# Kernel tuning notes

Measured on AMD Instinct MI355X. Metric: run time of the kernel, lower is better.

Reference implementation:

```python
import jax, jax.numpy as jnp
import numpy as np

EPS = 1e-7
BLOCK_SIZE = 128
LN_EPS = 1e-6

def _project(x):
    norm = jnp.maximum(jnp.linalg.norm(x, axis=-1, keepdims=True), EPS)
    max_norm = 1.0 - EPS
    return jnp.where(norm >= 1.0, x / norm * max_norm, x)

def _mobius_add(x, y, c):
    x2 = jnp.sum(x * x, -1, keepdims=True)
    y2 = jnp.sum(y * y, -1, keepdims=True)
    xy = jnp.sum(x * y, -1, keepdims=True)
    num = (1 + 2 * c * xy + c * y2) * x + (1 - c * x2) * y
    den = 1 + 2 * c * xy + c * c * x2 * y2
    return _project(num / jnp.maximum(den, EPS))

def _logmap0(y, c):
    sqrt_c = jnp.maximum(jnp.sqrt(c), EPS)
    y_norm = jnp.linalg.norm(y, axis=-1, keepdims=True)
    safe = jnp.maximum(y_norm, EPS)
    mag = jnp.arctanh(jnp.minimum(y_norm, 1.0 - EPS)) / sqrt_c
    return jnp.where(y_norm < EPS, jnp.zeros_like(y), mag * (y / safe))

def _expmap0(v, c):
    sqrt_c = jnp.maximum(jnp.sqrt(c), EPS)
    v_norm = jnp.linalg.norm(v, axis=-1, keepdims=True)
    safe = jnp.maximum(v_norm, EPS)
    mag = jnp.tanh(sqrt_c * safe) / sqrt_c
    return _project(jnp.where(v_norm < EPS, jnp.zeros_like(v), mag * (v / safe)))

def _dist(x, y, c):
    sqrt_c = jnp.maximum(jnp.sqrt(c), EPS)
    add_norm = jnp.linalg.norm(_mobius_add(-x, y, c), axis=-1)
    sc = jnp.squeeze(sqrt_c, -1)
    arg = jnp.minimum(sc * add_norm, 1.0 - EPS)
    return 2.0 * jnp.arctanh(arg) / sc

def _layernorm(t, scale, bias):
    mu = jnp.mean(t, -1, keepdims=True)
    var = jnp.mean((t - mu) ** 2, -1, keepdims=True)
    return (t - mu) * jax.lax.rsqrt(var + LN_EPS) * scale + bias

def _rope(x, fc):
    # x: [Be, H, bs, hd]; fc: [bs, hd//2] complex
    x_r, x_i = jnp.split(x, 2, -1)
    xc = jax.lax.complex(x_r, x_i)
    rot = xc * fc.reshape(1, 1, fc.shape[0], fc.shape[1])
    return jnp.concatenate([rot.real, rot.imag], -1)

def setup_inputs() -> dict:
    key = jax.random.key(0)
    ks = jax.random.split(key, 8)
    B, N, D, H = 1, 1024, 1024, 16
    w = lambda k, s: jax.random.normal(k, s, jnp.float32) * 0.02
    x = jax.random.normal(ks[0], (B, N, D), jnp.float32) * 0.02  # points inside the ball
    c_global = jax.random.uniform(ks[1], (B, 1), jnp.float32, minval=0.1, maxval=1.0)
    return dict(
        x=x, c_global=c_global,
        qkv_w=w(ks[2], (D, 3 * D)), qkv_b=jnp.zeros((3 * D,), jnp.float32),
        out_w=w(ks[3], (D, D)), out_b=jnp.zeros((D,), jnp.float32),
        ffn_w1=w(ks[4], (D, 4 * D)), ffn_b1=jnp.zeros((4 * D,), jnp.float32),
        ffn_w2=w(ks[5], (4 * D, D)), ffn_b2=jnp.zeros((D,), jnp.float32),
        ln1_scale=jnp.ones((D,), jnp.float32), ln1_bias=jnp.zeros((D,), jnp.float32),
        ln2_scale=jnp.ones((D,), jnp.float32), ln2_bias=jnp.zeros((D,), jnp.float32),
        c_logits=jnp.zeros((H,), jnp.float32),
        geo_scale=jnp.ones((1, H, 1, 1), jnp.float32),
        start_pos=0,
    )

def reference(x, c_global, qkv_w, qkv_b, out_w, out_b, ffn_w1, ffn_b1, ffn_w2, ffn_b2,
              ln1_scale, ln1_bias, ln2_scale, ln2_bias, c_logits, geo_scale, start_pos):
    B, N, D = x.shape
    H = c_logits.shape[0]
    hd = D // H
    bs = BLOCK_SIZE
    nb = N // bs
    Be = B * nb
    xb = x.reshape(Be, bs, D)
    c_b = jnp.repeat(c_global, nb, axis=0).reshape(Be, 1, 1)
    x_res1 = xb
    # tangent-space norm 1 + attention input
    x_norm = _expmap0(_layernorm(_logmap0(xb, c_b), ln1_scale, ln1_bias), c_b)
    x_tan = _logmap0(x_norm, c_b)
    qkv = (x_tan @ qkv_w + qkv_b).reshape(Be, bs, 3, H, hd).transpose(2, 0, 3, 1, 4)
    q, k, v = qkv[0], qkv[1], qkv[2]  # [Be, H, bs, hd]
    # block-local RoPE (module recomputes freqs_cis for h_dim/block_size internally)
    freqs = 1.0 / (10000.0 ** (jnp.arange(0, hd, 2, dtype=jnp.float32) / hd))
    fc = jnp.exp(1j * jnp.outer(jnp.arange(bs), freqs))
    q = _rope(q, fc)
    k = _rope(k, fc)
    c_head = jax.nn.softplus(c_logits).reshape(1, H, 1, 1)
    q_hyp = _expmap0(q, c_head)
    k_hyp = _expmap0(k, c_head)
    d = _dist(q_hyp[:, :, :, None, :], k_hyp[:, :, None, :, :], c_head[:, :, None, :, :])  # [Be,H,bs,bs]
    attn = jax.nn.softmax(-geo_scale * d, axis=-1)
    ao = jnp.einsum('bhqk,bhkd->bhqd', attn, v).transpose(0, 2, 1, 3).reshape(Be, bs, D)
    ao = ao @ out_w + out_b
    x_att = _mobius_add(x_res1, _expmap0(ao, c_b), c_b)
    # tangent-space norm 2 + hyperbolic FFN
    x_norm2 = _expmap0(_layernorm(_logmap0(x_att, c_b), ln2_scale, ln2_bias), c_b)
    t = _logmap0(x_norm2, c_b)
    t = jax.nn.gelu(t @ ffn_w1 + ffn_b1) @ ffn_w2 + ffn_b2
    x_ffn = _expmap0(t, c_b)
    out = _mobius_add(x_att, x_ffn, c_b)
    return out.reshape(B, N, D)
```

## Files before the change

kernel.cpp:

```cpp
#include <hip/hip_runtime.h>

typedef unsigned int uint;
typedef unsigned short ushort;
typedef __attribute__((ext_vector_type(8))) short bf16x8;
typedef __attribute__((ext_vector_type(4))) float f32x4;

#define EPSF 1e-7f
#define ONE_M_EPS 0.99999988079071044921875f
#define ATANH_1ME 8.4056213f
#define Y2_CLIP 0.99999982f

__device__ __forceinline__ ushort f2bf(float f){
  union{float f;uint u;}x; x.f=f; uint u=x.u;
  return (ushort)((u + 0x7fffu + ((u>>16)&1u)) >> 16);
}
__device__ __forceinline__ float bf2f(ushort u){
  union{uint u;float f;}x; x.u = ((uint)u)<<16; return x.f;
}
__device__ __forceinline__ float atanh_c(float a){
  a = fminf(a, ONE_M_EPS);
  return 0.5f*__logf((1.f+a)/(1.f-a));
}
__device__ __forceinline__ float gelu_t(float v){
  return 0.5f*v*(1.f + tanhf(0.7978845608f*(v + 0.044715f*v*v*v)));
}

__device__ __forceinline__ float expmap_factor(float n2, float sc, float& r2){
  float n = sqrtf(n2);
  if (n < EPSF) { r2 = 0.f; return 0.f; }
  float mag = tanhf(sc*n)/sc;
  float f = mag/n;
  if (mag >= 1.f) { f *= ONE_M_EPS/mag; r2 = Y2_CLIP; }
  else r2 = mag*mag;
  return f;
}
__device__ __forceinline__ float roundtrip_factor(float tn2, float sc){
  float tn = sqrtf(tn2);
  if (tn < EPSF) return 0.f;
  float mag = tanhf(sc*tn)/sc;
  if (mag >= 1.f) {
    return ATANH_1ME / (sc * tn);
  } else {
    if (mag < EPSF) return 0.f;
    return (mag/tn) * (atanh_c(mag) / (sc * mag));
  }
}

__device__ __constant__ float FREQS[32] = {
  1.0f, 0.7498942093324559f, 0.5623413251903491f, 0.4216965034285822f,
  0.31622776601683794f, 0.23713737056616552f, 0.1778279410038923f, 0.13335214321633242f,
  0.1f, 0.07498942093324558f, 0.05623413251903491f, 0.04216965034285822f,
  0.03162277660168379f, 0.023713737056616554f, 0.01778279410038923f, 0.013335214321633242f,
  0.01f, 0.007498942093324559f, 0.005623413251903491f, 0.004216965034285822f,
  0.0031622776601683794f, 0.0023713737056616554f, 0.0017782794100389228f, 0.0013335214321633241f,
  0.001f, 0.0007498942093324558f, 0.0005623413251903491f, 0.0004216965034285822f,
  0.00031622776601683794f, 0.00023713737056616553f, 0.00017782794100389227f, 0.00013335214321633243f
};

__device__ __forceinline__ float blkSum(float v, float* tmp){
  #pragma unroll
  for (int o=32;o>0;o>>=1) v += __shfl_xor(v, o, 64);
  int w = threadIdx.x >> 6;
  if ((threadIdx.x & 63) == 0) tmp[w] = v;
  __syncthreads();
  v = tmp[0]+tmp[1]+tmp[2]+tmp[3];
  __syncthreads();
  return v;
}
__device__ __forceinline__ float2 blkSum2(float a, float b, float* tmp){
  #pragma unroll
  for (int o=32;o>0;o>>=1){ a += __shfl_xor(a, o, 64); b += __shfl_xor(b, o, 64); }
  int w = threadIdx.x >> 6;
  if ((threadIdx.x & 63) == 0){ tmp[w] = a; tmp[4+w] = b; }
  __syncthreads();
  float2 r; r.x = tmp[0]+tmp[1]+tmp[2]+tmp[3]; r.y = tmp[4]+tmp[5]+tmp[6]+tmp[7];
  __syncthreads();
  return r;
}

__global__ __launch_bounds__(256) void k_pre(const float* __restrict__ qkv_w,
    const float* __restrict__ out_w, const float* __restrict__ ffn_w1,
    const float* __restrict__ ffn_w2, const float* __restrict__ x,
    const float* __restrict__ cg, const float* __restrict__ lns, const float* __restrict__ lnb,
    ushort* __restrict__ wq, ushort* __restrict__ wo,
    ushort* __restrict__ w1, ushort* __restrict__ w2, ushort* __restrict__ xtan){
  __shared__ float s[32][33];
  int b = blockIdx.x;
  if (b < 12288){
    const float* W; ushort* WT; int K, N;
    if (b < 3072){ W=qkv_w; WT=wq; K=1024; N=3072; }
    else if (b < 4096){ b-=3072; W=out_w; WT=wo; K=1024; N=1024; }
    else if (b < 8192){ b-=4096; W=ffn_w1; WT=w1; K=1024; N=4096; }
    else { b-=8192; W=ffn_w2; WT=w2; K=4096; N=1024; }
    int nbn = N >> 5;
    int n0 = (b % nbn)*32, k0 = (b / nbn)*32;
    int tx = threadIdx.x & 31, ty = threadIdx.x >> 5;
    #pragma unroll
    for (int i=0;i<4;i++)
      s[ty+8*i][tx] = W[(size_t)(k0+ty+8*i)*N + n0+tx];
    __syncthreads();
    #pragma unroll
    for (int i=0;i<4;i++)
      WT[(size_t)(n0+ty+8*i)*K + k0+tx] = f2bf(s[tx][ty+8*i]);
  } else {
    float* tmp = &s[0][0];
    int r = b - 12288, t = threadIdx.x;
    float c = cg[0];
    float sc = fmaxf(sqrtf(c), EPSF);
    float4 xv = ((const float4*)(x + (size_t)r*1024))[t];
    float n2 = blkSum(xv.x*xv.x + xv.y*xv.y + xv.z*xv.z + xv.w*xv.w, tmp);
    float n = sqrtf(n2);
    float f1 = (n < EPSF) ? 0.f : (atanh_c(n) / sc / n);
    float ux = xv.x*f1, uy = xv.y*f1, uz = xv.z*f1, uw = xv.w*f1;
    float2 s12 = blkSum2(ux+uy+uz+uw, ux*ux+uy*uy+uz*uz+uw*uw, tmp);
    float mu = s12.x*(1.f/1024.f);
    float var = s12.y*(1.f/1024.f) - mu*mu;
    float inv = rsqrtf(var + 1e-6f);
    float4 sv = ((const float4*)lns)[t];
    float4 bv = ((const float4*)lnb)[t];
    float ta = (ux-mu)*inv*sv.x + bv.x;
    float tb = (uy-mu)*inv*sv.y + bv.y;
    float tc = (uz-mu)*inv*sv.z + bv.z;
    float td = (uw-mu)*inv*sv.w + bv.w;
    float tn2 = blkSum(ta*ta+tb*tb+tc*tc+td*td, tmp);
    float f = roundtrip_factor(tn2, sc);
    ushort4 o; o.x=f2bf(ta*f); o.y=f2bf(tb*f); o.z=f2bf(tc*f); o.w=f2bf(td*f);
    ((ushort4*)(xtan + (size_t)r*1024))[t] = o;
  }
}

template<int EPI>
__global__ __launch_bounds__(256) void k_gemm(const ushort* __restrict__ A,
    const ushort* __restrict__ Bt, const float* __restrict__ bias,
    void* __restrict__ C, int M, int N, int Kstride, int Kchunk){
  constexpr int NF = 4;
  __shared__ ushort As[2][64*64];
  __shared__ ushort Bs[2][64*64];
  const int tid = threadIdx.x;
  const int lane = tid & 63;
  const int wid = tid >> 6;
  const int ro = wid * 16;
  const int l15 = lane & 15, hi = lane >> 4;
  const int nwg = gridDim.x * gridDim.y;
  const int lin = blockIdx.y * gridDim.x + blockIdx.x;
  const int qq = nwg >> 3, rr = nwg & 7;
  const int xcd = lin & 7, ii = lin >> 3;
  const int swz = (xcd < rr) ? (xcd*(qq+1) + ii) : (rr*(qq+1) + (xcd-rr)*qq + ii);
  const int m0 = (swz % gridDim.y) * 64;
  const int n0 = (swz / gridDim.y) * 64;
  const int z = blockIdx.z;
  const int kbase = z * Kchunk;
  const int swr = (l15 & 7) << 3;

  f32x4 acc[NF];
  #pragma unroll
  for (int j=0;j<NF;j++) acc[j] = (f32x4){0.f,0.f,0.f,0.f};

  auto stage = [&](int buf, int koff){
    #pragma unroll
    for (int r2=0;r2<2;r2++){
      int idx = r2*256 + tid;
      int row = idx >> 3, cc = idx & 7;
      int off = koff + ((cc ^ (row & 7)) << 3);
      int lo = (r2*256 + (tid & 192)) * 8;
      __builtin_amdgcn_global_load_lds((const __attribute__((address_space(1))) uint*)
          (A + (size_t)(m0+row)*Kstride + off),
          (__attribute__((address_space(3))) uint*)&As[buf][lo], 16, 0, 0);
      __builtin_amdgcn_global_load_lds((const __attribute__((address_space(1))) uint*)
          (Bt + (size_t)(n0+row)*Kstride + off),
          (__attribute__((address_space(3))) uint*)&Bs[buf][lo], 16, 0, 0);
    }
  };
  auto compute = [&](int buf){
    #pragma unroll
    for (int ks=0;ks<2;ks++){
      bf16x8 af, bfv[NF];
      int cb = (ks*32 + hi*8) ^ swr;
      af = *(const bf16x8*)&As[buf][(ro+l15)*64 + cb];
      #pragma unroll
      for (int n2=0;n2<NF;n2++) bfv[n2] = *(const bf16x8*)&Bs[buf][(n2*16+l15)*64 + cb];
      #pragma unroll
      for (int n2=0;n2<NF;n2++)
        acc[n2] = __builtin_amdgcn_mfma_f32_16x16x32_bf16(af, bfv[n2], acc[n2], 0, 0, 0);
    }
  };

  const int nt = Kchunk >> 6;
  stage(0, kbase);
  __syncthreads();
  int cur = 0;
  for (int t = 1; t < nt; ++t){
    stage(cur ^ 1, kbase + t*64);
    compute(cur);
    __syncthreads();
    cur ^= 1;
  }
  compute(cur);

  #pragma unroll
  for (int n=0;n<NF;n++){
    int gc = n0 + n*16 + l15;
    float bb = (EPI == 3) ? (z == 0 ? bias[gc] : 0.f) : bias[gc];
    #pragma unroll
    for (int i=0;i<4;i++){
      int gr = m0 + ro + hi*4 + i;
      float v = acc[n][i] + bb;
      if (EPI == 2) v = gelu_t(v);
      if (EPI == 2) ((ushort*)C)[(size_t)gr*N + gc] = f2bf(v);
      else ((float*)C)[(size_t)z*M*N + (size_t)gr*N + gc] = v;
    }
  }
}

__global__ __launch_bounds__(256) void k_qkvprep(const float* __restrict__ qkv,
    const float* __restrict__ clog,
    ushort* __restrict__ qhg, ushort* __restrict__ qlg,
    ushort* __restrict__ khg, ushort* __restrict__ klg,
    ushort* __restrict__ vhg, float* __restrict__ q2g, float* __restrict__ k2g){
  const int gr = blockIdx.x;
  const int be = gr >> 7, r = gr & 127;
  const int t = threadIdx.x;
  const int h = t >> 4, d = t & 15;
  const float cl = clog[h];
  const float ch = (cl > 20.f) ? cl : log1pf(__expf(cl));
  const float sc = fmaxf(sqrtf(ch), EPSF);
  const float* base = qkv + (size_t)gr*3072 + h*64;
  const size_t rowbase = ((size_t)(be*16 + h)*128 + r)*64;
  const float fr = (float)r;
  #pragma unroll
  for (int qk=0; qk<2; qk++){
    int off = qk*1024;
    float v0 = base[off+d];
    float v1 = base[off+d+16];
    float v2 = base[off+d+32];
    float v3 = base[off+d+48];
    float sn, cn;
    __sincosf(fr * FREQS[d], &sn, &cn);
    float a = v0, b = v2;
    v0 = a*cn - b*sn; v2 = a*sn + b*cn;
    __sincosf(fr * FREQS[d+16], &sn, &cn);
    a = v1; b = v3;
    v1 = a*cn - b*sn; v3 = a*sn + b*cn;
    float n2 = v0*v0 + v1*v1 + v2*v2 + v3*v3;
    #pragma unroll
    for (int o=1;o<16;o<<=1) n2 += __shfl_xor(n2, o);
    float r2; float f = expmap_factor(n2, sc, r2);
    ushort* hd = qk ? khg : qhg;
    ushort* ld = qk ? klg : qlg;
    float val;
    val = v0*f; ushort h0 = f2bf(val), l0 = f2bf(val - bf2f(h0));
    val = v1*f; ushort h1 = f2bf(val), l1 = f2bf(val - bf2f(h1));
    val = v2*f; ushort h2 = f2bf(val), l2 = f2bf(val - bf2f(h2));
    val = v3*f; ushort h3 = f2bf(val), l3 = f2bf(val - bf2f(h3));
    hd[rowbase+d]=h0; hd[rowbase+d+16]=h1; hd[rowbase+d+32]=h2; hd[rowbase+d+48]=h3;
    ld[rowbase+d]=l0; ld[rowbase+d+16]=l1; ld[rowbase+d+32]=l2; ld[rowbase+d+48]=l3;
    if (d == 0) (qk ? k2g : q2g)[(size_t)(be*16+h)*128 + r] = r2;
  }
  {
    vhg[rowbase+d]    = f2bf(base[2048+d]);
    vhg[rowbase+d+16] = f2bf(base[2048+d+16]);
    vhg[rowbase+d+32] = f2bf(base[2048+d+32]);
    vhg[rowbase+d+48] = f2bf(base[2048+d+48]);
  }
}

__global__ __launch_bounds__(256) void k_attn6(const ushort* __restrict__ qhg,
    const ushort* __restrict__ qlg, const ushort* __restrict__ khg,
    const ushort* __restrict__ klg, const ushort* __restrict__ vhg,
    const float* __restrict__ q2g, const float* __restrict__ k2g,
    const float* __restrict__ c_logits, const float* __restrict__ geo,
    ushort* __restrict__ ao){
  __shared__ ushort Kh[128*64], Kl[128*64];
  __shared__ ushort Vth[64*128];
  __shared__ ushort Qh[64*64], Ql[64*64];
  __shared__ float k2s[128], q2s[64];
  const int h = blockIdx.x, be = blockIdx.y, qs = blockIdx.z;
  const int tid = threadIdx.x;
  const float cl = c_logits[h];
  const float ch = (cl > 20.f) ? cl : log1pf(__expf(cl));
  const float sc = fmaxf(sqrtf(ch), EPSF);
  const float gs = geo[h];
  const size_t tbase = (size_t)(be*16 + h)*8192;

  #pragma unroll
  for (int r2=0;r2<4;r2++){
    int idx = r2*256 + tid;
    int row = idx >> 3, cc = idx & 7;
    int off = row*64 + ((cc ^ (row & 7)) << 3);
    int lo = (r2*256 + (tid & 192)) * 8;
    __builtin_amdgcn_global_load_lds((const __attribute__((address_space(1))) uint*)(khg + tbase + off),
        (__attribute__((address_space(3))) uint*)&Kh[lo], 16, 0, 0);
    __builtin_amdgcn_global_load_lds((const __attribute__((address_space(1))) uint*)(klg + tbase + off),
        (__attribute__((address_space(3))) uint*)&Kl[lo], 16, 0, 0);
  }
  #pragma unroll
  for (int r2=0;r2<2;r2++){
    int idx = r2*256 + tid;
    int row = idx >> 3, cc = idx & 7;
    int off = (qs*64 + row)*64 + ((cc ^ (row & 7)) << 3);
    int lo = (r2*256 + (tid & 192)) * 8;
    __builtin_amdgcn_global_load_lds((const __attribute__((address_space(1))) uint*)(qhg + tbase + off),
        (__attribute__((address_space(3))) uint*)&Qh[lo], 16, 0, 0);
    __builtin_amdgcn_global_load_lds((const __attribute__((address_space(1))) uint*)(qlg + tbase + off),
        (__attribute__((address_space(3))) uint*)&Ql[lo], 16, 0, 0);
  }
  if (tid < 128){
    int kv = tid;
    const uint4* src = (const uint4*)(vhg + tbase + kv*64);
    ushort v[64];
    #pragma unroll
    for (int c2=0;c2<8;c2++) *(uint4*)&v[c2*8] = src[c2];
    #pragma unroll
    for (int d=0; d<64; d++){
      int idx = d*128 + (((kv>>3) ^ (d&7))<<3) + (kv&7);
      Vth[idx] = v[d];
    }
    k2s[kv] = k2g[(size_t)(be*16+h)*128 + kv];
  } else if (tid < 192){
    int i2 = tid - 128;
    q2s[i2] = q2g[(size_t)(be*16+h)*128 + qs*64 + i2];
  }
  __syncthreads();

  const int lane = tid & 63, w = tid >> 6;
  const int l15 = lane & 15, hi4 = lane >> 4;
  f32x4 acc[8];
  #pragma unroll
  for (int nf=0;nf<8;nf++) acc[nf] = (f32x4){0.f,0.f,0.f,0.f};
  #pragma unroll
  for (int ks=0; ks<2; ks++){
    int qrowL = w*16 + l15;
    int qidx = qrowL*64 + (((ks*4 + hi4) ^ (qrowL&7))<<3);
    bf16x8 qh = *(const bf16x8*)&Qh[qidx];
    bf16x8 ql2 = *(const bf16x8*)&Ql[qidx];
    #pragma unroll
    for (int nf=0; nf<8; nf++){
      int krow = nf*16 + l15;
      int kidx = krow*64 + (((ks*4 + hi4) ^ (krow&7))<<3);
      bf16x8 kh = *(const bf16x8*)&Kh[kidx];
      bf16x8 kl2 = *(const bf16x8*)&Kl[kidx];
      acc[nf] = __builtin_amdgcn_mfma_f32_16x16x32_bf16(qh, kh, acc[nf], 0, 0, 0);
      acc[nf] = __builtin_amdgcn_mfma_f32_16x16x32_bf16(qh, kl2, acc[nf], 0, 0, 0);
      acc[nf] = __builtin_amdgcn_mfma_f32_16x16x32_bf16(ql2, kh, acc[nf], 0, 0, 0);
    }
  }
  __syncthreads();

  float q2v[4], Bfv[4];
  #pragma unroll
  for (int i=0;i<4;i++){ q2v[i] = q2s[w*16 + hi4*4 + i]; Bfv[i] = 1.f - ch*q2v[i]; }
  const float e2 = 2.f*ch;
  #pragma unroll
  for (int nf=0; nf<8; nf++){
    float k2 = k2s[nf*16 + l15];
    #pragma unroll
    for (int i=0;i<4;i++){
      float xy = acc[nf][i];
      float Af = 1.f + ch*k2 - e2*xy;
      float den = fmaxf(Af - ch*k2*Bfv[i], EPSF);
      float num2 = fmaxf(Af*(Af*q2v[i] - 2.f*Bfv[i]*xy) + Bfv[i]*Bfv[i]*k2, 0.f);
      float rn = sqrtf(num2)/den;
      rn = (rn >= 1.f) ? ONE_M_EPS : rn;
      float arg = fminf(sc*rn, ONE_M_EPS);
      float dd = __logf((1.f+arg)/(1.f-arg)) / sc;
      acc[nf][i] = -gs*dd;
    }
  }
  #pragma unroll
  for (int i=0;i<4;i++){
    float m = acc[0][i];
    #pragma unroll
    for (int nf=1;nf<8;nf++) m = fmaxf(m, acc[nf][i]);
    #pragma unroll
    for (int o=1;o<16;o<<=1) m = fmaxf(m, __shfl_xor(m, o));
    float l = 0.f;
    #pragma unroll
    for (int nf=0;nf<8;nf++){ float pp = __expf(acc[nf][i]-m); acc[nf][i] = pp; l += pp; }
    #pragma unroll
    for (int o=1;o<16;o<<=1) l += __shfl_xor(l, o);
    float inv = 1.f/l;
    #pragma unroll
    for (int nf=0;nf<8;nf++){
      float p = acc[nf][i]*inv;
      ushort ph = f2bf(p);
      ushort pl = f2bf(p - bf2f(ph));
      int row = w*16 + hi4*4 + i, col = nf*16 + l15;
      int idx = row*128 + (((col>>3) ^ (row&7))<<3) + (col&7);
      Kh[idx] = ph; Kl[idx] = pl;
    }
  }
  __syncthreads();

  f32x4 acc2[4];
  #pragma unroll
  for (int nf=0;nf<4;nf++) acc2[nf] = (f32x4){0.f,0.f,0.f,0.f};
  #pragma unroll
  for (int ks=0; ks<4; ks++){
    int prow = w*16 + l15;
    int pidx = prow*128 + (((ks*4 + hi4) ^ (prow&7))<<3);
    bf16x8 ph = *(const bf16x8*)&Kh[pidx];
    bf16x8 pl = *(const bf16x8*)&Kl[pidx];
    #pragma unroll
    for (int nf=0; nf<4; nf++){
      int vrow = nf*16 + l15;
      int vidx = vrow*128 + (((ks*4 + hi4) ^ (vrow&7))<<3);
      bf16x8 vh = *(const bf16x8*)&Vth[vidx];
      acc2[nf] = __builtin_amdgcn_mfma_f32_16x16x32_bf16(ph, vh, acc2[nf], 0, 0, 0);
      acc2[nf] = __builtin_amdgcn_mfma_f32_16x16x32_bf16(pl, vh, acc2[nf], 0, 0, 0);
    }
  }
  #pragma unroll
  for (int nf=0; nf<4; nf++)
    #pragma unroll
    for (int i=0;i<4;i++){
      int row = qs*64 + w*16 + hi4*4 + i;
      int col = nf*16 + l15;
      ao[(size_t)(be*128 + row)*1024 + h*64 + col] = f2bf(acc2[nf][i]);
    }
}

__global__ __launch_bounds__(256) void k_postattn(const float* __restrict__ x,
    const float* __restrict__ proj, const float* __restrict__ cg,
    const float* __restrict__ lns, const float* __restrict__ lnb,
    float* __restrict__ xatt, ushort* __restrict__ tout){
  __shared__ float tmp[8];
  int r = blockIdx.x, t = threadIdx.x;
  float c = cg[0], sc = fmaxf(sqrtf(c), EPSF);
  float4 pa = ((const float4*)(proj + (size_t)r*1024))[t];
  float4 pb = ((const float4*)(proj + 1024*1024 + (size_t)r*1024))[t];
  float4 pc = ((const float4*)(proj + 2*1024*1024 + (size_t)r*1024))[t];
  float4 pd = ((const float4*)(proj + 3*1024*1024 + (size_t)r*1024))[t];
  float4 pv; pv.x=(pa.x+pb.x)+(pc.x+pd.x); pv.y=(pa.y+pb.y)+(pc.y+pd.y);
  pv.z=(pa.z+pb.z)+(pc.z+pd.z); pv.w=(pa.w+pb.w)+(pc.w+pd.w);
  float4 xv = ((const float4*)(x + (size_t)r*1024))[t];
  float pn2 = blkSum(pv.x*pv.x+pv.y*pv.y+pv.z*pv.z+pv.w*pv.w, tmp);
  float y2; float fy = expmap_factor(pn2, sc, y2);
  float ya = pv.x*fy, yb = pv.y*fy, yc = pv.z*fy, yd = pv.w*fy;
  float2 s = blkSum2(xv.x*xv.x+xv.y*xv.y+xv.z*xv.z+xv.w*xv.w,
                     xv.x*ya+xv.y*yb+xv.z*yc+xv.w*yd, tmp);
  float x2 = s.x, xy = s.y;
  float Af = 1.f + 2.f*c*xy + c*y2;
  float Bf = 1.f - c*x2;
  float den = fmaxf(1.f + 2.f*c*xy + c*c*x2*y2, EPSF);
  float num2 = fmaxf(Af*Af*x2 + 2.f*Af*Bf*xy + Bf*Bf*y2, 0.f);
  float rn = sqrtf(num2)/den;
  float fp = (rn >= 1.f) ? (ONE_M_EPS/fmaxf(rn,EPSF)) : 1.f;
  float xan = (rn >= 1.f) ? ONE_M_EPS : rn;
  float g = fp/den;
  float xa = (Af*xv.x + Bf*ya)*g;
  float xb = (Af*xv.y + Bf*yb)*g;
  float xc = (Af*xv.z + Bf*yc)*g;
  float xd = (Af*xv.w + Bf*yd)*g;
  float4 xo; xo.x=xa; xo.y=xb; xo.z=xc; xo.w=xd;
  ((float4*)(xatt + (size_t)r*1024))[t] = xo;
  float at = (rn >= 1.f) ? ATANH_1ME : atanh_c(xan);
  float fl = (xan < EPSF) ? 0.f : at / sc / fmaxf(xan, EPSF);
  float ux = xa*fl, uy = xb*fl, uz = xc*fl, uw = xd*fl;
  float2 s12 = blkSum2(ux+uy+uz+uw, ux*ux+uy*uy+uz*uz+uw*uw, tmp);
  float mu = s12.x*(1.f/1024.f);
  float var = s12.y*(1.f/1024.f) - mu*mu;
  float inv = rsqrtf(var + 1e-6f);
  float4 sv = ((const float4*)lns)[t];
  float4 bv = ((const float4*)lnb)[t];
  float ta = (ux-mu)*inv*sv.x + bv.x;
  float tb = (uy-mu)*inv*sv.y + bv.y;
  float tc = (uz-mu)*inv*sv.z + bv.z;
  float td = (uw-mu)*inv*sv.w + bv.w;
  float tn2 = blkSum(ta*ta+tb*tb+tc*tc+td*td, tmp);
  float f = roundtrip_factor(tn2, sc);
  ushort4 o; o.x=f2bf(ta*f); o.y=f2bf(tb*f); o.z=f2bf(tc*f); o.w=f2bf(td*f);
  ((ushort4*)(tout + (size_t)r*1024))[t] = o;
}

__global__ __launch_bounds__(256) void k_final(const float* __restrict__ xatt,
    const float* __restrict__ tf, const float* __restrict__ cg, float* __restrict__ out){
  __shared__ float tmp[8];
  int r = blockIdx.x, t = threadIdx.x;
  float c = cg[0], sc = fmaxf(sqrtf(c), EPSF);
  float4 fa = ((const float4*)(tf + (size_t)r*1024))[t];
  float4 fb = ((const float4*)(tf + 1024*1024 + (size_t)r*1024))[t];
  float4 fc = ((const float4*)(tf + 2*1024*1024 + (size_t)r*1024))[t];
  float4 fd = ((const float4*)(tf + 3*1024*1024 + (size_t)r*1024))[t];
  float4 fv; fv.x=(fa.x+fb.x)+(fc.x+fd.x); fv.y=(fa.y+fb.y)+(fc.y+fd.y);
  fv.z=(fa.z+fb.z)+(fc.z+fd.z); fv.w=(fa.w+fb.w)+(fc.w+fd.w);
  float4 xv = ((const float4*)(xatt + (size_t)r*1024))[t];
  float fn2 = blkSum(fv.x*fv.x+fv.y*fv.y+fv.z*fv.z+fv.w*fv.w, tmp);
  float y2; float fy = expmap_factor(fn2, sc, y2);
  float ya = fv.x*fy, yb = fv.y*fy, yc = fv.z*fy, yd = fv.w*fy;
  float2 s = blkSum2(xv.x*xv.x+xv.y*xv.y+xv.z*xv.z+xv.w*xv.w,
                     xv.x*ya+xv.y*yb+xv.z*yc+xv.w*yd, tmp);
  float x2 = s.x, xy = s.y;
  float Af = 1.f + 2.f*c*xy + c*y2;
  float Bf = 1.f - c*x2;
  float den = fmaxf(1.f + 2.f*c*xy + c*c*x2*y2, EPSF);
  float num2 = fmaxf(Af*Af*x2 + 2.f*Af*Bf*xy + Bf*Bf*y2, 0.f);
  float rn = sqrtf(num2)/den;
  float fp = (rn >= 1.f) ? (ONE_M_EPS/fmaxf(rn,EPSF)) : 1.f;
  float g = fp/den;
  float4 o;
  o.x = (Af*xv.x + Bf*ya)*g;
  o.y = (Af*xv.y + Bf*yb)*g;
  o.z = (Af*xv.z + Bf*yc)*g;
  o.w = (Af*xv.w + Bf*yd)*g;
  ((float4*)(out + (size_t)r*1024))[t] = o;
}

extern "C" void kernel_launch(void* const* d_in, const int* in_sizes, int n_in,
                              void* d_out, int out_size, void* d_ws, size_t ws_size,
                              hipStream_t stream){
  (void)in_sizes; (void)n_in; (void)out_size; (void)ws_size;
  const float* x     = (const float*)d_in[0];
  const float* cg    = (const float*)d_in[1];
  const float* qkv_w = (const float*)d_in[2];
  const float* qkv_b = (const float*)d_in[3];
  const float* out_w = (const float*)d_in[4];
  const float* out_b = (const float*)d_in[5];
  const float* ffn_w1= (const float*)d_in[6];
  const float* ffn_b1= (const float*)d_in[7];
  const float* ffn_w2= (const float*)d_in[8];
  const float* ffn_b2= (const float*)d_in[9];
  const float* ln1s  = (const float*)d_in[10];
  const float* ln1b  = (const float*)d_in[11];
  const float* ln2s  = (const float*)d_in[12];
  const float* ln2b  = (const float*)d_in[13];
  const float* clog  = (const float*)d_in[14];
  const float* geo   = (const float*)d_in[15];

  char* p = (char*)d_ws;
  auto take = [&](size_t n){ char* r = p; p += (n + 255) & ~(size_t)255; return r; };
  ushort* wt_qkv  = (ushort*)take((size_t)3072*1024*2);
  ushort* wt_out  = (ushort*)take((size_t)1024*1024*2);
  ushort* wt_ffn1 = (ushort*)take((size_t)4096*1024*2);
  ushort* wt_ffn2 = (ushort*)take((size_t)1024*4096*2);
  float*  bufA    = (float*)take((size_t)1024*3072*4);
  ushort* bufB    = (ushort*)take((size_t)1024*1024*2);
  float*  bufC    = (float*)take((size_t)4*1024*1024*4);
  float*  xatt    = (float*)take((size_t)1024*1024*4);
  ushort* tbuf    = (ushort*)take((size_t)1024*1024*2);
  ushort* qhg     = (ushort*)take((size_t)1024*1024*2);
  ushort* qlg     = (ushort*)take((size_t)1024*1024*2);
  ushort* khg     = (ushort*)take((size_t)1024*1024*2);
  ushort* klg     = (ushort*)take((size_t)1024*1024*2);
  ushort* vhg     = (ushort*)take((size_t)1024*1024*2);
  float*  q2g     = (float*)take((size_t)16384*4);
  float*  k2g     = (float*)take((size_t)16384*4);

  k_pre<<<13312, 256, 0, stream>>>(qkv_w, out_w, ffn_w1, ffn_w2, x, cg, ln1s, ln1b,
                                   wt_qkv, wt_out, wt_ffn1, wt_ffn2, bufB);
  k_gemm<3><<<dim3(48,16,1), 256, 0, stream>>>(bufB, wt_qkv, qkv_b, (void*)bufA, 1024, 3072, 1024, 1024);
  k_qkvprep<<<1024, 256, 0, stream>>>(bufA, clog, qhg, qlg, khg, klg, vhg, q2g, k2g);
  k_attn6<<<dim3(16,8,2), 256, 0, stream>>>(qhg, qlg, khg, klg, vhg, q2g, k2g, clog, geo, bufB);
  k_gemm<3><<<dim3(16,16,4), 256, 0, stream>>>(bufB, wt_out, out_b, (void*)bufC, 1024, 1024, 1024, 256);
  k_postattn<<<1024, 256, 0, stream>>>(x, bufC, cg, ln2s, ln2b, xatt, tbuf);
  k_gemm<2><<<dim3(64,16,1), 256, 0, stream>>>(tbuf, wt_ffn1, ffn_b1, (void*)bufA, 1024, 4096, 1024, 1024);
  k_gemm<3><<<dim3(16,16,4), 256, 0, stream>>>((const ushort*)bufA, wt_ffn2, ffn_b2, (void*)bufC, 1024, 1024, 4096, 1024);
  k_final<<<1024, 256, 0, stream>>>(xatt, bufC, cg, (float*)d_out);
}
```

Baseline: 113.3 us.

## Fuse QKV RoPE/expmap/bf16 split epilogue into QKV GEMM, drop qkvprep kernel

Adds a GEMM epilogue variant that applies RoPE, the expmap0 scaling, the hi/lo bf16 split and the head-major scatter directly from the accumulators, then deletes the separate k_qkvprep kernel. This avoids writing and re-reading the 12 MB fp32 QKV intermediate and saves one kernel launch. In exchange the GEMM epilogue gets heavier, with per-row sincos and cross-lane shuffles, and its scattered 2-byte stores may coalesce poorly. The bufA allocation is enlarged, though that does not appear needed for this path.

```diff
diff --git a/kernel.cpp b/kernel.cpp
--- a/kernel.cpp
+++ b/kernel.cpp
@@ -132,7 +132,11 @@
 template<int EPI>
 __global__ __launch_bounds__(256) void k_gemm(const ushort* __restrict__ A,
     const ushort* __restrict__ Bt, const float* __restrict__ bias,
-    void* __restrict__ C, int M, int N, int Kstride, int Kchunk){
+    void* __restrict__ C, int M, int N, int Kstride, int Kchunk,
+    ushort* __restrict__ qhg = nullptr, ushort* __restrict__ qlg = nullptr,
+    ushort* __restrict__ khg = nullptr, ushort* __restrict__ klg = nullptr,
+    ushort* __restrict__ vhg = nullptr, float* __restrict__ q2g = nullptr,
+    float* __restrict__ k2g = nullptr, const float* __restrict__ clog = nullptr){
   constexpr int NF = 4;
   __shared__ ushort As[2][64*64];
   __shared__ ushort Bs[2][64*64];
@@ -197,6 +201,64 @@
   }
   compute(cur);
 
+  if (EPI == 4){
+    const int type = n0 >> 10;
+    const int h = (n0 & 1023) >> 6;
+    float v[NF][4];
+    #pragma unroll
+    for (int n2=0;n2<NF;n2++){
+      float bb = bias[n0 + n2*16 + l15];
+      #pragma unroll
+      for (int i=0;i<4;i++) v[n2][i] = acc[n2][i] + bb;
+    }
+    if (type < 2){
+      const float cl = clog[h];
+      const float chh = (cl > 20.f) ? cl : log1pf(__expf(cl));
+      const float sch = fmaxf(sqrtf(chh), EPSF);
+      ushort* hdst = (type==0) ? qhg : khg;
+      ushort* ldst = (type==0) ? qlg : klg;
+      float*  sdst = (type==0) ? q2g : k2g;
+      #pragma unroll
+      for (int i=0;i<4;i++){
+        int gr = m0 + ro + hi*4 + i;
+        int r = gr & 127, be = gr >> 7;
+        float fr = (float)r;
+        float sn, cn;
+        __sincosf(fr * FREQS[l15], &sn, &cn);
+        float a = v[0][i], b = v[2][i];
+        v[0][i] = a*cn - b*sn; v[2][i] = a*sn + b*cn;
+        __sincosf(fr * FREQS[l15+16], &sn, &cn);
+        a = v[1][i]; b = v[3][i];
+        v[1][i] = a*cn - b*sn; v[3][i] = a*sn + b*cn;
+        float n2s = v[0][i]*v[0][i] + v[1][i]*v[1][i] + v[2][i]*v[2][i] + v[3][i]*v[3][i];
+        #pragma unroll
+        for (int o=1;o<16;o<<=1) n2s += __shfl_xor(n2s, o);
+        float r2; float f = expmap_factor(n2s, sch, r2);
+        size_t rowbase = ((size_t)(be*16 + h)*128 + r)*64;
+        #pragma unroll
+        for (int n2=0;n2<NF;n2++){
+          float val = v[n2][i]*f;
+          ushort hb = f2bf(val);
+          ushort lb = f2bf(val - bf2f(hb));
+          hdst[rowbase + n2*16 + l15] = hb;
+          ldst[rowbase + n2*16 + l15] = lb;
+        }
+        if (l15 == 0) sdst[(size_t)(be*16+h)*128 + r] = r2;
+      }
+    } else {
+      #pragma unroll
+      for (int i=0;i<4;i++){
+        int gr = m0 + ro + hi*4 + i;
+        int r = gr & 127, be = gr >> 7;
+        size_t rowbase = ((size_t)(be*16 + h)*128 + r)*64;
+        #pragma unroll
+        for (int n2=0;n2<NF;n2++)
+          vhg[rowbase + n2*16 + l15] = f2bf(v[n2][i]);
+      }
+    }
+    return;
+  }
+
   #pragma unroll
   for (int n=0;n<NF;n++){
     int gc = n0 + n*16 + l15;
@@ -209,58 +271,6 @@
       if (EPI == 2) ((ushort*)C)[(size_t)gr*N + gc] = f2bf(v);
       else ((float*)C)[(size_t)z*M*N + (size_t)gr*N + gc] = v;
     }
-  }
-}
-
-__global__ __launch_bounds__(256) void k_qkvprep(const float* __restrict__ qkv,
-    const float* __restrict__ clog,
-    ushort* __restrict__ qhg, ushort* __restrict__ qlg,
-    ushort* __restrict__ khg, ushort* __restrict__ klg,
-    ushort* __restrict__ vhg, float* __restrict__ q2g, float* __restrict__ k2g){
-  const int gr = blockIdx.x;
-  const int be = gr >> 7, r = gr & 127;
-  const int t = threadIdx.x;
-  const int h = t >> 4, d = t & 15;
-  const float cl = clog[h];
-  const float ch = (cl > 20.f) ? cl : log1pf(__expf(cl));
-  const float sc = fmaxf(sqrtf(ch), EPSF);
-  const float* base = qkv + (size_t)gr*3072 + h*64;
-  const size_t rowbase = ((size_t)(be*16 + h)*128 + r)*64;
-  const float fr = (float)r;
-  #pragma unroll
-  for (int qk=0; qk<2; qk++){
-    int off = qk*1024;
-    float v0 = base[off+d];
-    float v1 = base[off+d+16];
-    float v2 = base[off+d+32];
-    float v3 = base[off+d+48];
-    float sn, cn;
-    __sincosf(fr * FREQS[d], &sn, &cn);
-    float a = v0, b = v2;
-    v0 = a*cn - b*sn; v2 = a*sn + b*cn;
-    __sincosf(fr * FREQS[d+16], &sn, &cn);
-    a = v1; b = v3;
-    v1 = a*cn - b*sn; v3 = a*sn + b*cn;
-    float n2 = v0*v0 + v1*v1 + v2*v2 + v3*v3;
-    #pragma unroll
-    for (int o=1;o<16;o<<=1) n2 += __shfl_xor(n2, o);
-    float r2; float f = expmap_factor(n2, sc, r2);
-    ushort* hd = qk ? khg : qhg;
-    ushort* ld = qk ? klg : qlg;
-    float val;
-    val = v0*f; ushort h0 = f2bf(val), l0 = f2bf(val - bf2f(h0));
-    val = v1*f; ushort h1 = f2bf(val), l1 = f2bf(val - bf2f(h1));
-    val = v2*f; ushort h2 = f2bf(val), l2 = f2bf(val - bf2f(h2));
-    val = v3*f; ushort h3 = f2bf(val), l3 = f2bf(val - bf2f(h3));
-    hd[rowbase+d]=h0; hd[rowbase+d+16]=h1; hd[rowbase+d+32]=h2; hd[rowbase+d+48]=h3;
-    ld[rowbase+d]=l0; ld[rowbase+d+16]=l1; ld[rowbase+d+32]=l2; ld[rowbase+d+48]=l3;
-    if (d == 0) (qk ? k2g : q2g)[(size_t)(be*16+h)*128 + r] = r2;
-  }
-  {
-    vhg[rowbase+d]    = f2bf(base[2048+d]);
-    vhg[rowbase+d+16] = f2bf(base[2048+d+16]);
-    vhg[rowbase+d+32] = f2bf(base[2048+d+32]);
-    vhg[rowbase+d+48] = f2bf(base[2048+d+48]);
   }
 }
 
@@ -532,7 +542,7 @@
   ushort* wt_out  = (ushort*)take((size_t)1024*1024*2);
   ushort* wt_ffn1 = (ushort*)take((size_t)4096*1024*2);
   ushort* wt_ffn2 = (ushort*)take((size_t)1024*4096*2);
-  float*  bufA    = (float*)take((size_t)1024*3072*4);
+  float*  bufA    = (float*)take((size_t)1024*4096*4);
   ushort* bufB    = (ushort*)take((size_t)1024*1024*2);
   float*  bufC    = (float*)take((size_t)4*1024*1024*4);
   float*  xatt    = (float*)take((size_t)1024*1024*4);
@@ -547,8 +557,8 @@
 
   k_pre<<<13312, 256, 0, stream>>>(qkv_w, out_w, ffn_w1, ffn_w2, x, cg, ln1s, ln1b,
                                    wt_qkv, wt_out, wt_ffn1, wt_ffn2, bufB);
-  k_gemm<3><<<dim3(48,16,1), 256, 0, stream>>>(bufB, wt_qkv, qkv_b, (void*)bufA, 1024, 3072, 1024, 1024);
-  k_qkvprep<<<1024, 256, 0, stream>>>(bufA, clog, qhg, qlg, khg, klg, vhg, q2g, k2g);
+  k_gemm<4><<<dim3(48,16,1), 256, 0, stream>>>(bufB, wt_qkv, qkv_b, nullptr, 1024, 3072, 1024, 1024,
+                                               qhg, qlg, khg, klg, vhg, q2g, k2g, clog);
   k_attn6<<<dim3(16,8,2), 256, 0, stream>>>(qhg, qlg, khg, klg, vhg, q2g, k2g, clog, geo, bufB);
   k_gemm<3><<<dim3(16,16,4), 256, 0, stream>>>(bufB, wt_out, out_b, (void*)bufC, 1024, 1024, 1024, 256);
   k_postattn<<<1024, 256, 0, stream>>>(x, bufC, cg, ln2s, ln2b, xatt, tbuf);
```

After: 110.9 us, median of 2. -2.1%, faster.
